# Performance work log

Hardware: AMD Instinct MI355X
Metric: run time of the kernel (lower is better)

The kernel has to match this reference:

```python
import jax, jax.numpy as jnp
import numpy as np
from jax import lax

BETA = 0.95
THRESH = 1.0
NUM_INPUTS, NUM_HIDDEN, NUM_CLASSES, NUM_STEPS, BATCH = 80, 256, 2, 200, 4096


@jax.custom_vjp
def spike_fn(x):
    # Heaviside spike; surrogate gradient = fast_sigmoid (slope=25)
    return (x > 0).astype(x.dtype)

def _spike_fwd(x):
    return spike_fn(x), x

def _spike_bwd(x, g):
    slope = 25.0
    return (g / (slope * jnp.abs(x) + 1.0) ** 2,)

spike_fn.defvjp(_spike_fwd, _spike_bwd)


def _linear_init(key, fan_in, fan_out):
    # torch nn.Linear default init: U(-1/sqrt(fan_in), 1/sqrt(fan_in))
    k1, k2 = jax.random.split(key)
    bound = 1.0 / np.sqrt(fan_in)
    W = jax.random.uniform(k1, (fan_out, fan_in), jnp.float32, -bound, bound)
    b = jax.random.uniform(k2, (fan_out,), jnp.float32, -bound, bound)
    return W, b


def setup_inputs() -> dict:
    key = jax.random.key(0)
    kx, k1, k2, k3, k4 = jax.random.split(key, 5)
    x = jax.random.normal(kx, (BATCH, NUM_INPUTS, NUM_STEPS), jnp.float32)
    W1, b1 = _linear_init(k1, NUM_INPUTS, NUM_HIDDEN)
    W2, b2 = _linear_init(k2, NUM_HIDDEN, NUM_HIDDEN)
    W3, b3 = _linear_init(k3, NUM_HIDDEN, NUM_HIDDEN)
    W4, b4 = _linear_init(k4, NUM_HIDDEN, NUM_CLASSES)
    return {"x": x, "W1": W1, "b1": b1, "W2": W2, "b2": b2,
            "W3": W3, "b3": b3, "W4": W4, "b4": b4}


def _lif(cur, mem):
    # snntorch Leaky, reset_mechanism='subtract': reset from previous mem (detached)
    reset = lax.stop_gradient((mem > THRESH).astype(mem.dtype))
    mem = BETA * mem + cur - reset * THRESH
    spk = spike_fn(mem - THRESH)
    return spk, mem


def reference(x, W1, b1, W2, b2, W3, b3, W4, b4):
    B = x.shape[0]
    xt = jnp.transpose(x, (2, 0, 1))  # [T, B, 80]
    m1 = jnp.zeros((B, NUM_HIDDEN), x.dtype)
    m2 = jnp.zeros((B, NUM_HIDDEN), x.dtype)
    m3 = jnp.zeros((B, NUM_HIDDEN), x.dtype)
    m4 = jnp.zeros((B, NUM_CLASSES), x.dtype)

    def step(carry, x_t):
        m1, m2, m3, m4 = carry
        s1, m1 = _lif(x_t @ W1.T + b1, m1)
        s2, m2 = _lif(s1 @ W2.T + b2, m2)
        s3, m3 = _lif(s2 @ W3.T + b3, m3)
        s4, m4 = _lif(s3 @ W4.T + b4, m4)
        return (m1, m2, m3, m4), s4

    _, spk4_rec = lax.scan(step, (m1, m2, m3, m4), xt)
    return spk4_rec  # [T, B, num_classes]
```

## Files before the change

kernel.cpp:

```cpp
#include <hip/hip_runtime.h>
#include <cstddef>


#define BATCH 4096
#define TSTEPS 200
#define NIN 80
#define KP 96
#define NH 256
#define XPAD 104
#define SPAD 264

#define W1HI 0
#define W1LO 24576
#define W2HI 49152
#define W2LO 114688
#define W3HI 180224
#define W3LO 245760

#define LO_SCALE 2048.0f
#define LO_INV 4.8828125e-4f

typedef _Float16 h8 __attribute__((ext_vector_type(8)));
typedef float f4 __attribute__((ext_vector_type(4)));

__global__ __launch_bounds__(256) void prep_kernel(
    const float* __restrict__ W1, const float* __restrict__ W2,
    const float* __restrict__ W3, _Float16* __restrict__ ws) {
  unsigned id = blockIdx.x * 256u + threadIdx.x;
  if (id >= 24576u + 65536u + 65536u) return;
  float v;
  unsigned off;
  _Float16 *hi, *lo;
  if (id < 24576u) {
    unsigned n = id / KP, k = id % KP;
    v = (k < NIN) ? W1[n * NIN + k] : 0.0f;
    hi = ws + W1HI; lo = ws + W1LO; off = id;
  } else if (id < 90112u) {
    off = id - 24576u; v = W2[off];
    hi = ws + W2HI; lo = ws + W2LO;
  } else {
    off = id - 90112u; v = W3[off];
    hi = ws + W3HI; lo = ws + W3LO;
  }
  _Float16 h = (_Float16)v;
  float r = (v - (float)h) * LO_SCALE;
  hi[off] = h;
  lo[off] = (_Float16)r;
}

__global__ __launch_bounds__(1024) void snn_kernel(
    const float* __restrict__ x,
    const float* __restrict__ b1, const float* __restrict__ b2,
    const float* __restrict__ b3, const float* __restrict__ W4,
    const float* __restrict__ b4, const _Float16* __restrict__ ws,
    float* __restrict__ out) {
  __shared__ alignas(16) _Float16 xAhi[4][16][XPAD];
  __shared__ alignas(16) _Float16 xAlo[4][16][XPAD];
  __shared__ alignas(16) _Float16 S1[16][SPAD];
  __shared__ alignas(16) _Float16 S2[16][SPAD];
  __shared__ alignas(16) _Float16 S3[16][SPAD];

  const int tid = threadIdx.x;
  const int wave = tid >> 6;
  const int lane = tid & 63;
  const int n16 = lane & 15;
  const int kg = lane >> 4;
  const int wb = blockIdx.x << 4;
  const int nb = wave << 4;
  const int nn = nb + n16;

  const _Float16* w1h = ws + W1HI + nn * KP;
  const _Float16* w1l = ws + W1LO + nn * KP;
  const _Float16* w2h = ws + W2HI + nn * NH;
  const _Float16* w2l = ws + W2LO + nn * NH;
  const _Float16* w3h = ws + W3HI + nn * NH;
  const _Float16* w3l = ws + W3LO + nn * NH;

  const float bb1 = b1[nn], bb2 = b2[nn], bb3 = b3[nn];

  const int j4 = lane >> 5;
  const int ks4 = (lane & 31) << 3;
  float w4r[8];
#pragma unroll
  for (int u = 0; u < 8; ++u) w4r[u] = W4[j4 * NH + ks4 + u];
  const float bb4 = b4[j4];

  float mem1[4] = {0.f, 0.f, 0.f, 0.f};
  float mem2[4] = {0.f, 0.f, 0.f, 0.f};
  float mem3[4] = {0.f, 0.f, 0.f, 0.f};
  float mem4 = 0.f;

  for (int t = 0; t < TSTEPS; ++t) {
    const int ph = t & 3;
    if (ph == 0) {
      for (unsigned e = (unsigned)tid; e < 16u * KP; e += 1024u) {
        unsigned m = e / KP, i = e % KP;
        f4 v = {0.f, 0.f, 0.f, 0.f};
        if (i < NIN)
          v = *(const f4*)(x + ((size_t)(wb + m) * NIN + i) * TSTEPS + t);
#pragma unroll
        for (int s = 0; s < 4; ++s) {
          float f = v[s];
          _Float16 h = (_Float16)f;
          xAhi[s][m][i] = h;
          xAlo[s][m][i] = (_Float16)((f - (float)h) * LO_SCALE);
        }
      }
      __syncthreads();
    }

    f4 aH = {0.f, 0.f, 0.f, 0.f};
    f4 aL = {0.f, 0.f, 0.f, 0.f};
#pragma unroll
    for (int kt = 0; kt < 3; ++kt) {
      const int ko = kt * 32 + kg * 8;
      h8 ahi = *(const h8*)&xAhi[ph][n16][ko];
      h8 alo = *(const h8*)&xAlo[ph][n16][ko];
      h8 whi = *(const h8*)(w1h + ko);
      h8 wlo = *(const h8*)(w1l + ko);
      aH = __builtin_amdgcn_mfma_f32_16x16x32_f16(ahi, whi, aH, 0, 0, 0);
      aL = __builtin_amdgcn_mfma_f32_16x16x32_f16(alo, whi, aL, 0, 0, 0);
      aL = __builtin_amdgcn_mfma_f32_16x16x32_f16(ahi, wlo, aL, 0, 0, 0);
    }
#pragma unroll
    for (int r = 0; r < 4; ++r) {
      float cur = __fadd_rn(__fadd_rn(aH[r], __fmul_rn(aL[r], LO_INV)), bb1);
      float mo = mem1[r];
      float mn = __fsub_rn(__fadd_rn(__fmul_rn(0.95f, mo), cur),
                           (mo > 1.0f) ? 1.0f : 0.0f);
      mem1[r] = mn;
      S1[kg * 4 + r][nn] = (mn > 1.0f) ? (_Float16)1.0f : (_Float16)0.0f;
    }
    __syncthreads();

    aH = (f4){0.f, 0.f, 0.f, 0.f};
    aL = (f4){0.f, 0.f, 0.f, 0.f};
#pragma unroll
    for (int kt = 0; kt < 8; ++kt) {
      const int ko = kt * 32 + kg * 8;
      h8 a = *(const h8*)&S1[n16][ko];
      h8 whi = *(const h8*)(w2h + ko);
      h8 wlo = *(const h8*)(w2l + ko);
      aH = __builtin_amdgcn_mfma_f32_16x16x32_f16(a, whi, aH, 0, 0, 0);
      aL = __builtin_amdgcn_mfma_f32_16x16x32_f16(a, wlo, aL, 0, 0, 0);
    }
#pragma unroll
    for (int r = 0; r < 4; ++r) {
      float cur = __fadd_rn(__fadd_rn(aH[r], __fmul_rn(aL[r], LO_INV)), bb2);
      float mo = mem2[r];
      float mn = __fsub_rn(__fadd_rn(__fmul_rn(0.95f, mo), cur),
                           (mo > 1.0f) ? 1.0f : 0.0f);
      mem2[r] = mn;
      S2[kg * 4 + r][nn] = (mn > 1.0f) ? (_Float16)1.0f : (_Float16)0.0f;
    }
    __syncthreads();

    aH = (f4){0.f, 0.f, 0.f, 0.f};
    aL = (f4){0.f, 0.f, 0.f, 0.f};
#pragma unroll
    for (int kt = 0; kt < 8; ++kt) {
      const int ko = kt * 32 + kg * 8;
      h8 a = *(const h8*)&S2[n16][ko];
      h8 whi = *(const h8*)(w3h + ko);
      h8 wlo = *(const h8*)(w3l + ko);
      aH = __builtin_amdgcn_mfma_f32_16x16x32_f16(a, whi, aH, 0, 0, 0);
      aL = __builtin_amdgcn_mfma_f32_16x16x32_f16(a, wlo, aL, 0, 0, 0);
    }
#pragma unroll
    for (int r = 0; r < 4; ++r) {
      float cur = __fadd_rn(__fadd_rn(aH[r], __fmul_rn(aL[r], LO_INV)), bb3);
      float mo = mem3[r];
      float mn = __fsub_rn(__fadd_rn(__fmul_rn(0.95f, mo), cur),
                           (mo > 1.0f) ? 1.0f : 0.0f);
      mem3[r] = mn;
      S3[kg * 4 + r][nn] = (mn > 1.0f) ? (_Float16)1.0f : (_Float16)0.0f;
    }
    __syncthreads();

    {
      h8 s = *(const h8*)&S3[wave][ks4];
      float p = 0.0f;
#pragma unroll
      for (int u = 0; u < 8; ++u)
        p = __fadd_rn(p, __fmul_rn((float)s[u], w4r[u]));
#pragma unroll
      for (int msk = 1; msk <= 16; msk <<= 1)
        p = __fadd_rn(p, __shfl_xor(p, msk));
      float cur = __fadd_rn(p, bb4);
      float mo = mem4;
      float mn = __fsub_rn(__fadd_rn(__fmul_rn(0.95f, mo), cur),
                           (mo > 1.0f) ? 1.0f : 0.0f);
      mem4 = mn;
      if ((lane & 31) == 0)
        out[(size_t)t * (BATCH * 2) + (size_t)(wb + wave) * 2 + j4] =
            (mn > 1.0f) ? 1.0f : 0.0f;
    }
  }
}

extern "C" void kernel_launch(void* const* d_in, const int* in_sizes, int n_in,
                              void* d_out, int out_size, void* d_ws,
                              size_t ws_size, hipStream_t stream) {
  const float* x  = (const float*)d_in[0];
  const float* W1 = (const float*)d_in[1];
  const float* b1 = (const float*)d_in[2];
  const float* W2 = (const float*)d_in[3];
  const float* b2 = (const float*)d_in[4];
  const float* W3 = (const float*)d_in[5];
  const float* b3 = (const float*)d_in[6];
  const float* W4 = (const float*)d_in[7];
  const float* b4 = (const float*)d_in[8];
  float* out = (float*)d_out;
  _Float16* ws = (_Float16*)d_ws;

  hipLaunchKernelGGL(prep_kernel, dim3(608), dim3(256), 0, stream,
                     W1, W2, W3, ws);
  hipLaunchKernelGGL(snn_kernel, dim3(BATCH / 16), dim3(1024), 0, stream,
                     x, b1, b2, b3, W4, b4, ws, out);
}
```

Baseline: 3.126 ms.

## Keep W2/W3 high halves in registers and use LDS-only barriers

Loads the fp16 high parts of W2 and W3 into registers once before the time loop, so they are no longer re-read from global/L2 every step. Low parts are batch-loaded in groups of four ahead of their MFMAs, and W1 loads are hoisted ahead of the LDS reads. __syncthreads is replaced by a barrier that waits only on LDS counters, so pending global work no longer stalls it. This adds 64 VGPRs per thread at 1024 threads per block, which risks spilling or reduced occupancy.

```diff
diff --git a/kernel.cpp b/kernel.cpp
--- a/kernel.cpp
+++ b/kernel.cpp
@@ -22,6 +22,11 @@
 
 typedef _Float16 h8 __attribute__((ext_vector_type(8)));
 typedef float f4 __attribute__((ext_vector_type(4)));
+
+__device__ __forceinline__ void lds_barrier() {
+  __builtin_amdgcn_s_waitcnt(0xC07F);
+  __builtin_amdgcn_s_barrier();
+}
 
 __global__ __launch_bounds__(256) void prep_kernel(
     const float* __restrict__ W1, const float* __restrict__ W2,
@@ -66,17 +71,25 @@
   const int n16 = lane & 15;
   const int kg = lane >> 4;
   const int wb = blockIdx.x << 4;
-  const int nb = wave << 4;
-  const int nn = nb + n16;
+  const int nn = (wave << 4) + n16;
 
   const _Float16* w1h = ws + W1HI + nn * KP;
   const _Float16* w1l = ws + W1LO + nn * KP;
-  const _Float16* w2h = ws + W2HI + nn * NH;
   const _Float16* w2l = ws + W2LO + nn * NH;
-  const _Float16* w3h = ws + W3HI + nn * NH;
   const _Float16* w3l = ws + W3LO + nn * NH;
 
   const float bb1 = b1[nn], bb2 = b2[nn], bb3 = b3[nn];
+
+  h8 w2hi_r[8], w3hi_r[8];
+  {
+    const _Float16* w2h = ws + W2HI + nn * NH;
+    const _Float16* w3h = ws + W3HI + nn * NH;
+#pragma unroll
+    for (int kt = 0; kt < 8; ++kt) {
+      w2hi_r[kt] = *(const h8*)(w2h + kt * 32 + kg * 8);
+      w3hi_r[kt] = *(const h8*)(w3h + kt * 32 + kg * 8);
+    }
+  }
 
   const int j4 = lane >> 5;
   const int ks4 = (lane & 31) << 3;
@@ -106,21 +119,27 @@
           xAlo[s][m][i] = (_Float16)((f - (float)h) * LO_SCALE);
         }
       }
-      __syncthreads();
+      lds_barrier();
     }
 
     f4 aH = {0.f, 0.f, 0.f, 0.f};
     f4 aL = {0.f, 0.f, 0.f, 0.f};
-#pragma unroll
-    for (int kt = 0; kt < 3; ++kt) {
-      const int ko = kt * 32 + kg * 8;
-      h8 ahi = *(const h8*)&xAhi[ph][n16][ko];
-      h8 alo = *(const h8*)&xAlo[ph][n16][ko];
-      h8 whi = *(const h8*)(w1h + ko);
-      h8 wlo = *(const h8*)(w1l + ko);
-      aH = __builtin_amdgcn_mfma_f32_16x16x32_f16(ahi, whi, aH, 0, 0, 0);
-      aL = __builtin_amdgcn_mfma_f32_16x16x32_f16(alo, whi, aL, 0, 0, 0);
-      aL = __builtin_amdgcn_mfma_f32_16x16x32_f16(ahi, wlo, aL, 0, 0, 0);
+    {
+      h8 wh[3], wl[3];
+#pragma unroll
+      for (int kt = 0; kt < 3; ++kt) {
+        wh[kt] = *(const h8*)(w1h + kt * 32 + kg * 8);
+        wl[kt] = *(const h8*)(w1l + kt * 32 + kg * 8);
+      }
+#pragma unroll
+      for (int kt = 0; kt < 3; ++kt) {
+        const int ko = kt * 32 + kg * 8;
+        h8 ahi = *(const h8*)&xAhi[ph][n16][ko];
+        h8 alo = *(const h8*)&xAlo[ph][n16][ko];
+        aH = __builtin_amdgcn_mfma_f32_16x16x32_f16(ahi, wh[kt], aH, 0, 0, 0);
+        aL = __builtin_amdgcn_mfma_f32_16x16x32_f16(alo, wh[kt], aL, 0, 0, 0);
+        aL = __builtin_amdgcn_mfma_f32_16x16x32_f16(ahi, wl[kt], aL, 0, 0, 0);
+      }
     }
 #pragma unroll
     for (int r = 0; r < 4; ++r) {
@@ -131,18 +150,23 @@
       mem1[r] = mn;
       S1[kg * 4 + r][nn] = (mn > 1.0f) ? (_Float16)1.0f : (_Float16)0.0f;
     }
-    __syncthreads();
+    lds_barrier();
 
     aH = (f4){0.f, 0.f, 0.f, 0.f};
     aL = (f4){0.f, 0.f, 0.f, 0.f};
 #pragma unroll
-    for (int kt = 0; kt < 8; ++kt) {
-      const int ko = kt * 32 + kg * 8;
-      h8 a = *(const h8*)&S1[n16][ko];
-      h8 whi = *(const h8*)(w2h + ko);
-      h8 wlo = *(const h8*)(w2l + ko);
-      aH = __builtin_amdgcn_mfma_f32_16x16x32_f16(a, whi, aH, 0, 0, 0);
-      aL = __builtin_amdgcn_mfma_f32_16x16x32_f16(a, wlo, aL, 0, 0, 0);
+    for (int g = 0; g < 2; ++g) {
+      h8 wl[4];
+#pragma unroll
+      for (int q = 0; q < 4; ++q)
+        wl[q] = *(const h8*)(w2l + (g * 4 + q) * 32 + kg * 8);
+#pragma unroll
+      for (int q = 0; q < 4; ++q) {
+        const int kt = g * 4 + q;
+        h8 a = *(const h8*)&S1[n16][kt * 32 + kg * 8];
+        aH = __builtin_amdgcn_mfma_f32_16x16x32_f16(a, w2hi_r[kt], aH, 0, 0, 0);
+        aL = __builtin_amdgcn_mfma_f32_16x16x32_f16(a, wl[q], aL, 0, 0, 0);
+      }
     }
 #pragma unroll
     for (int r = 0; r < 4; ++r) {
@@ -153,18 +177,23 @@
       mem2[r] = mn;
       S2[kg * 4 + r][nn] = (mn > 1.0f) ? (_Float16)1.0f : (_Float16)0.0f;
     }
-    __syncthreads();
+    lds_barrier();
 
     aH = (f4){0.f, 0.f, 0.f, 0.f};
     aL = (f4){0.f, 0.f, 0.f, 0.f};
 #pragma unroll
-    for (int kt = 0; kt < 8; ++kt) {
-      const int ko = kt * 32 + kg * 8;
-      h8 a = *(const h8*)&S2[n16][ko];
-      h8 whi = *(const h8*)(w3h + ko);
-      h8 wlo = *(const h8*)(w3l + ko);
-      aH = __builtin_amdgcn_mfma_f32_16x16x32_f16(a, whi, aH, 0, 0, 0);
-      aL = __builtin_amdgcn_mfma_f32_16x16x32_f16(a, wlo, aL, 0, 0, 0);
+    for (int g = 0; g < 2; ++g) {
+      h8 wl[4];
+#pragma unroll
+      for (int q = 0; q < 4; ++q)
+        wl[q] = *(const h8*)(w3l + (g * 4 + q) * 32 + kg * 8);
+#pragma unroll
+      for (int q = 0; q < 4; ++q) {
+        const int kt = g * 4 + q;
+        h8 a = *(const h8*)&S2[n16][kt * 32 + kg * 8];
+        aH = __builtin_amdgcn_mfma_f32_16x16x32_f16(a, w3hi_r[kt], aH, 0, 0, 0);
+        aL = __builtin_amdgcn_mfma_f32_16x16x32_f16(a, wl[q], aL, 0, 0, 0);
+      }
     }
 #pragma unroll
     for (int r = 0; r < 4; ++r) {
@@ -175,7 +204,7 @@
       mem3[r] = mn;
       S3[kg * 4 + r][nn] = (mn > 1.0f) ? (_Float16)1.0f : (_Float16)0.0f;
     }
-    __syncthreads();
+    lds_barrier();
 
     {
       h8 s = *(const h8*)&S3[wave][ks4];
```

Measured after the change: 3.009 ms. -3.8%, faster.
